# Performance work log

Hardware: AMD Instinct MI355X
Metric: run time of the kernel (lower is better)

Reference implementation:

```python
import jax, jax.numpy as jnp
import numpy as np

B, S, DIM = 2, 2048, 4096
N_HEADS, N_KV_HEADS = 32, 8
HEAD_DIM = DIM // N_HEADS  # 128
N_REP = N_HEADS // N_KV_HEADS  # 4
NEG_INF = -1e9


def setup_inputs() -> dict:
    key = jax.random.key(0)
    ks = jax.random.split(key, 6)
    x = jax.random.normal(ks[0], (B, S, DIM), dtype=jnp.float32)
    # torch Linear weights are [out_features, in_features]
    sc = 0.02
    wq = jax.random.normal(ks[1], (N_HEADS * HEAD_DIM, DIM), dtype=jnp.float32) * sc
    wk = jax.random.normal(ks[2], (N_KV_HEADS * HEAD_DIM, DIM), dtype=jnp.float32) * sc
    wv = jax.random.normal(ks[3], (N_KV_HEADS * HEAD_DIM, DIM), dtype=jnp.float32) * sc
    wo = jax.random.normal(ks[4], (DIM, N_HEADS * HEAD_DIM), dtype=jnp.float32) * sc
    # RoPE frequencies, matching llama precompute_freqs_cis (theta=10000)
    inv = 1.0 / (10000.0 ** (np.arange(0, HEAD_DIM, 2, dtype=np.float32) / HEAD_DIM))
    t = np.arange(S, dtype=np.float32)
    freqs = np.outer(t, inv)  # [S, HEAD_DIM//2]
    freqs_cos = jnp.asarray(np.cos(freqs), dtype=jnp.float32)
    freqs_sin = jnp.asarray(np.sin(freqs), dtype=jnp.float32)
    # causal mask: 0 on/below diagonal, large negative above
    mask = jnp.triu(jnp.full((S, S), NEG_INF, dtype=jnp.float32), k=1)
    return {"x": x, "wq": wq, "wk": wk, "wv": wv, "wo": wo,
            "freqs_cos": freqs_cos, "freqs_sin": freqs_sin,
            "mask": mask, "start_pos": 0}


def _apply_rope(t, cos, sin):
    # t: [b, s, h, hd]; complex mult on interleaved (even, odd) pairs
    tr, ti = t[..., 0::2], t[..., 1::2]
    cos = cos[None, :, None, :]
    sin = sin[None, :, None, :]
    out_r = tr * cos - ti * sin
    out_i = tr * sin + ti * cos
    return jnp.stack([out_r, out_i], axis=-1).reshape(t.shape)


def reference(x, wq, wk, wv, wo, freqs_cos, freqs_sin, mask, start_pos):
    bsz, seqlen, _ = x.shape
    xq = (x @ wq.T).reshape(bsz, seqlen, N_HEADS, HEAD_DIM)
    xk = (x @ wk.T).reshape(bsz, seqlen, N_KV_HEADS, HEAD_DIM)
    xv = (x @ wv.T).reshape(bsz, seqlen, N_KV_HEADS, HEAD_DIM)
    xq = _apply_rope(xq, freqs_cos, freqs_sin)
    xk = _apply_rope(xk, freqs_cos, freqs_sin)
    # prefill: start_pos == 0, so cache slice == current keys/values
    # GQA repeat_kv via broadcast (torch repeat_interleave over head dim)
    keys = jnp.broadcast_to(xk[:, :, :, None, :],
                            (bsz, seqlen, N_KV_HEADS, N_REP, HEAD_DIM)
                            ).reshape(bsz, seqlen, N_HEADS, HEAD_DIM)
    values = jnp.broadcast_to(xv[:, :, :, None, :],
                              (bsz, seqlen, N_KV_HEADS, N_REP, HEAD_DIM)
                              ).reshape(bsz, seqlen, N_HEADS, HEAD_DIM)
    scale = 1.0 / jnp.sqrt(jnp.float32(HEAD_DIM))
    # [b, h, q, k]
    scores = jnp.einsum('bqhd,bkhd->bhqk', xq, keys) * scale
    scores = scores + mask[None, None, :, :]
    probs = jax.nn.softmax(scores.astype(jnp.float32), axis=-1).astype(xq.dtype)
    out = jnp.einsum('bhqk,bkhd->bqhd', probs, values)
    out = out.reshape(bsz, seqlen, N_HEADS * HEAD_DIM)
    return out @ wo.T
```

## Files before the change

### kernel.cpp

```cpp
#include <hip/hip_runtime.h>

typedef unsigned short u16;
typedef unsigned int u32;
typedef __bf16 bf16_t;
typedef bf16_t bf16x8 __attribute__((ext_vector_type(8)));
typedef float f32x4 __attribute__((ext_vector_type(4)));

#define B_ 2
#define S_ 2048
#define DIM_ 4096
#define NH_ 32
#define NKV_ 8
#define HD_ 128

__device__ __forceinline__ u16 f2b(float f) {
  union { float f; unsigned u; } x; x.f = f;
  unsigned r = x.u + 0x7fffu + ((x.u >> 16) & 1u);
  return (u16)(r >> 16);
}
__device__ __forceinline__ float b2f(u16 u) {
  union { unsigned u; float f; } x; x.u = ((unsigned)u) << 16;
  return x.f;
}
__device__ __forceinline__ u32 cvtpk(float lo, float hi) {
  u32 r;
  asm volatile("v_cvt_pk_bf16_f32 %0, %1, %2" : "=v"(r) : "v"(lo), "v"(hi));
  return r;
}
__device__ __forceinline__ float redmax4(float x) {
  x = fmaxf(x, __shfl_xor(x, 16));
  x = fmaxf(x, __shfl_xor(x, 32));
  return x;
}
__device__ __forceinline__ float redsum4(float x) {
  x += __shfl_xor(x, 16);
  x += __shfl_xor(x, 32);
  return x;
}

#define GLDS(gsrc, ldst) \
  __builtin_amdgcn_global_load_lds((const __attribute__((address_space(1))) void*)(gsrc), \
                                   (__attribute__((address_space(3))) void*)(ldst), 16, 0, 0)
#define BAR()    __builtin_amdgcn_s_barrier()
#define SCHED0() __builtin_amdgcn_sched_barrier(0)

__global__ void cvt_kernel(const float* __restrict__ in, u16* __restrict__ out, int n4) {
  int i = blockIdx.x * blockDim.x + threadIdx.x;
  int stride = gridDim.x * blockDim.x;
  for (; i < n4; i += stride) {
    float4 v = ((const float4*)in)[i];
    ushort4 o;
    o.x = f2b(v.x); o.y = f2b(v.y); o.z = f2b(v.z); o.w = f2b(v.w);
    ((ushort4*)out)[i] = o;
  }
}

__global__ void rope_kernel(u16* __restrict__ t, const float* __restrict__ fc,
                            const float* __restrict__ fs, int nheads) {
  int idx = blockIdx.x * blockDim.x + threadIdx.x;
  int ppr = nheads * 64;
  int row = idx / ppr;
  int pr = idx - row * ppr;
  int h = pr >> 6, j = pr & 63;
  int s = row & (S_ - 1);
  float c = fc[s * 64 + j], sn = fs[s * 64 + j];
  u16* p = t + (size_t)row * (size_t)(nheads * HD_) + h * HD_ + j * 2;
  float tr = b2f(p[0]), ti = b2f(p[1]);
  p[0] = f2b(tr * c - ti * sn);
  p[1] = f2b(tr * sn + ti * c);
}

template<int MODE, bool SM>
__global__ __launch_bounds__(512, 2) void gemm256(const u16* __restrict__ A,
                                                  const u16* __restrict__ B,
                                                  void* __restrict__ Cout,
                                                  void* __restrict__ Cout2,
                                                  int M, int N, int K) {
  constexpr int BM = SM ? 128 : 256;
  constexpr int AH = SM ? 4096 : 8192;
  constexpr int II = SM ? 1 : 2;
  constexpr int NACC = SM ? 4 : 8;
  __shared__ u16 As[2][2][AH];
  __shared__ u16 Bs[2][2][8192];
  const int nbn = N >> 8;
  const int nwg = gridDim.x;
  int wg = blockIdx.x;
  wg = (wg & 7) * (nwg >> 3) + (wg >> 3);
  const int bm = wg / nbn;
  const int bn = wg - bm * nbn;
  const int tid = threadIdx.x;
  const int lane = tid & 63;
  const int wv = tid >> 6;
  const int wm = wv >> 2, wn = wv & 3;
  const int qloc = lane & 15, grp = lane >> 4;
  const int NT = K >> 6;

  f32x4 acc[NACC][4];
#pragma unroll
  for (int i = 0; i < NACC; i++)
#pragma unroll
    for (int j = 0; j < 4; j++)
#pragma unroll
      for (int r = 0; r < 4; r++) acc[i][j][r] = 0.0f;

  const int srowl = lane >> 3;
  const int scsw = 8 * ((lane & 7) ^ srowl);
  const size_t rowA = SM ? ((size_t)(bm * 128 + wv * 8 + srowl) * K + scsw)
                         : ((size_t)(bm * 256 + wv * 16 + srowl) * K + scsw);
  const size_t rowB = (size_t)(bn * 256 + wv * 16 + srowl) * K + scsw;

#define STAGE_A(buf, h, tt) { \
    if (SM) { \
      GLDS(A + rowA + (size_t)((h) * 64) * K + (size_t)(tt) * 64, &As[buf][h][wv * 512]); \
    } else { \
      GLDS(A + rowA + (size_t)((h) * 128) * K + (size_t)(tt) * 64, &As[buf][h][wv * 1024]); \
      GLDS(A + rowA + (size_t)((h) * 128 + 8) * K + (size_t)(tt) * 64, &As[buf][h][wv * 1024 + 512]); } }
#define STAGE_B(buf, h, tt) { \
    GLDS(B + rowB + (size_t)((h) * 128) * K + (size_t)(tt) * 64, &Bs[buf][h][wv * 1024]); \
    GLDS(B + rowB + (size_t)((h) * 128 + 8) * K + (size_t)(tt) * 64, &Bs[buf][h][wv * 1024 + 512]); }

  STAGE_A(0, 0, 0); STAGE_A(0, 1, 0);
  STAGE_B(0, 0, 0); STAGE_B(0, 1, 0);
  STAGE_B(1, 0, 1); STAGE_B(1, 1, 1);
  asm volatile("s_waitcnt vmcnt(4)" ::: "memory");
  BAR();

  for (int t = 0; t < NT; t += 2) {
#pragma unroll
    for (int half = 0; half < 2; half++) {
      bf16x8 bfr[4][2];
#pragma unroll
      for (int qd = 0; qd < 4; qd++) {
        if (qd == 0) {
#pragma unroll
          for (int j = 0; j < 4; j++)
#pragma unroll
            for (int ks = 0; ks < 2; ks++) {
              int rb = (wn & 1) * 64 + j * 16 + qloc;
              bfr[j][ks] = *(const bf16x8*)((const char*)&Bs[half][wn >> 1][0]
                           + rb * 128 + ((ks * 64 + grp * 16) ^ ((rb & 7) << 4)));
            }
        }
        bf16x8 af[II][2];
#pragma unroll
        for (int ii = 0; ii < II; ii++)
#pragma unroll
          for (int ks = 0; ks < 2; ks++) {
            int rh = SM ? (qd * 16 + qloc) : (qd * 32 + ii * 16 + qloc);
            af[ii][ks] = *(const bf16x8*)((const char*)&As[half][wm][0]
                         + rh * 128 + ((ks * 64 + grp * 16) ^ ((rh & 7) << 4)));
          }
        const int ph = half * 4 + qd;
        if (ph == 0)      { STAGE_A(1, 0, t + 1); }
        else if (ph == 1) { STAGE_A(1, 1, t + 1); }
        else if (ph == 2) { if (t + 2 < NT) STAGE_B(0, 0, t + 2); }
        else if (ph == 3) { if (t + 2 < NT) STAGE_B(0, 1, t + 2); }
        else if (ph == 4) { if (t + 2 < NT) STAGE_A(0, 0, t + 2); }
        else if (ph == 5) { if (t + 2 < NT) STAGE_A(0, 1, t + 2); }
        else if (ph == 6) { if (t + 3 < NT) STAGE_B(1, 0, t + 3); }
        else              { if (t + 3 < NT) STAGE_B(1, 1, t + 3); }
        BAR();
        __builtin_amdgcn_s_setprio(1);
#pragma unroll
        for (int ii = 0; ii < II; ii++)
#pragma unroll
          for (int ks = 0; ks < 2; ks++)
#pragma unroll
            for (int j = 0; j < 4; j++)
              acc[qd * II + ii][j] = __builtin_amdgcn_mfma_f32_16x16x32_bf16(
                  af[ii][ks], bfr[j][ks], acc[qd * II + ii][j], 0, 0, 0);
        __builtin_amdgcn_s_setprio(0);
        SCHED0();
        if (qd == 3) {
          if ((half == 0 ? t + 2 : t + 3) < NT)
            asm volatile("s_waitcnt vmcnt(4)" ::: "memory");
          else
            asm volatile("s_waitcnt vmcnt(0)" ::: "memory");
        }
        BAR();
      }
    }
  }
#undef STAGE_A
#undef STAGE_B

  const int r0g = bm * BM + wm * (BM / 2) + grp * 4;
  const int c0g = bn * 256 + wn * 64 + qloc;
#pragma unroll
  for (int i = 0; i < NACC; i++)
#pragma unroll
    for (int j = 0; j < 4; j++)
#pragma unroll
      for (int r = 0; r < 4; r++) {
        int row = r0g + i * 16 + r;
        int col = c0g + j * 16;
        float v = acc[i][j][r];
        if (MODE == 1)      ((float*)Cout)[(size_t)row * N + col] = v;
        else if (MODE == 0) ((u16*)Cout)[(size_t)row * N + col]  = f2b(v);
        else {
          if (col < 1024) ((u16*)Cout)[(size_t)row * 1024 + col] = f2b(v);
          else            ((u16*)Cout2)[(size_t)(col - 1024) * M + row] = f2b(v);
        }
      }
}

__global__ __launch_bounds__(512) void attn_kernel(const u16* __restrict__ Q,
                                                   const u16* __restrict__ Kt,
                                                   const u16* __restrict__ VT,
                                                   u16* __restrict__ O,
                                                   const float* __restrict__ fc,
                                                   const float* __restrict__ fs) {
  __shared__ u16 Ks[2][32 * 128];
  __shared__ u16 Vs[2][32 * 128];

  const int bid = blockIdx.x;
  const int qb = 15 - (bid >> 6);
  const int h = bid & 31;
  const int b = (bid >> 5) & 1;
  const int g = h >> 2;
  const int tid = threadIdx.x;
  const int lane = tid & 63;
  const int wv = tid >> 6;
  const int qrow0 = qb * 128 + wv * 16;
  const float scl2 = 0.12751744f;

  const int qloc = lane & 15;
  const int grp = lane >> 4;

  bf16x8 qf[4];
  {
    const int qr = qrow0 + qloc;
    const u16* qptr = Q + (size_t)(b * S_ + qr) * (NH_ * HD_) + h * HD_ + grp * 8;
#pragma unroll
    for (int c = 0; c < 4; c++) {
      union { bf16x8 v; u16 u[8]; } raw;
      raw.v = *(const bf16x8*)(qptr + c * 32);
      const int p0 = c * 16 + grp * 4;
      const float4 cv = *(const float4*)&fc[(size_t)qr * 64 + p0];
      const float4 sv = *(const float4*)&fs[(size_t)qr * 64 + p0];
      union { bf16x8 v; u32 w[4]; } out;
      const float cc[4] = {cv.x, cv.y, cv.z, cv.w};
      const float ss[4] = {sv.x, sv.y, sv.z, sv.w};
#pragma unroll
      for (int j = 0; j < 4; j++) {
        float tr = b2f(raw.u[2 * j]), ti = b2f(raw.u[2 * j + 1]);
        out.w[j] = cvtpk(tr * cc[j] - ti * ss[j], tr * ss[j] + ti * cc[j]);
      }
      qf[c] = out.v;
    }
  }

  float m = -1e30f, l = 0.f;
  f32x4 o[8];
#pragma unroll
  for (int c = 0; c < 8; c++)
#pragma unroll
    for (int r = 0; r < 4; r++) o[c][r] = 0.f;

  const int nkv = 4 * qb + 4;

  int ka[2][4];
#pragma unroll
  for (int n = 0; n < 2; n++)
#pragma unroll
    for (int c = 0; c < 4; c++) {
      int krow = n * 16 + qloc;
      ka[n][c] = krow * 256 + ((c * 64 + grp * 16) ^ ((krow & 7) << 4));
    }
  int va[8];
#pragma unroll
  for (int c = 0; c < 8; c++) {
    int d = c * 16 + qloc;
    va[c] = d * 64 + ((grp * 16) ^ (((d >> 1) & 3) << 4));
  }

  const int kkey = wv * 4 + grp;
  const int cbsK = (qloc * 16) ^ ((kkey & 7) << 4);
  const int vd = wv * 16 + (lane >> 2);
  const int kbsV = ((lane & 3) * 16) ^ (((vd >> 1) & 3) << 4);

  const u16* kp = Kt + (size_t)(b * S_ + kkey) * 1024 + g * HD_ + (cbsK >> 1);
  const u16* vp = VT + (size_t)(g * HD_ + vd) * 4096 + (size_t)b * S_ + (kbsV >> 1);

  GLDS(kp, &Ks[0][wv * 512]);
  GLDS(vp, &Vs[0][wv * 512]);
  kp += 32 * 1024;
  vp += 32;

#define ATTN_ITER(T, CB, NB)                                                   \
  {                                                                            \
    const bool pf = ((T) + 1 < nkv);                                           \
    if (pf) {                                                                  \
      GLDS(kp, &Ks[NB][wv * 512]);                                             \
      GLDS(vp, &Vs[NB][wv * 512]);                                             \
      asm volatile("s_waitcnt vmcnt(2)" ::: "memory");                         \
    } else {                                                                   \
      asm volatile("s_waitcnt vmcnt(0)" ::: "memory");                         \
    }                                                                          \
    BAR();                                                                     \
    SCHED0();                                                                  \
    if ((T) * 32 <= qrow0 + 15) {                                              \
      f32x4 s[2];                                                              \
      __builtin_amdgcn_s_setprio(1);                                           \
      _Pragma("unroll")                                                        \
      for (int n = 0; n < 2; n++) {                                            \
        f32x4 sc;                                                              \
        _Pragma("unroll")                                                      \
        for (int r = 0; r < 4; r++) sc[r] = 0.f;                               \
        _Pragma("unroll")                                                      \
        for (int c = 0; c < 4; c++) {                                          \
          bf16x8 kf = *(const bf16x8*)((const char*)Ks[CB] + ka[n][c]);        \
          sc = __builtin_amdgcn_mfma_f32_16x16x32_bf16(kf, qf[c], sc, 0, 0, 0);\
        }                                                                      \
        s[n] = sc;                                                             \
      }                                                                        \
      __builtin_amdgcn_s_setprio(0);                                           \
      const int q = qrow0 + qloc;                                              \
      if ((T) * 32 + 31 > qrow0) {                                             \
        _Pragma("unroll")                                                      \
        for (int n = 0; n < 2; n++)                                            \
          _Pragma("unroll")                                                    \
          for (int r = 0; r < 4; r++) {                                        \
            int k = (T) * 32 + n * 16 + grp * 4 + r;                           \
            if (k > q) s[n][r] = -1e9f;                                        \
          }                                                                    \
      }                                                                        \
      float pmax = fmaxf(fmaxf(fmaxf(s[0][0], s[0][1]), fmaxf(s[0][2], s[0][3])), \
                         fmaxf(fmaxf(s[1][0], s[1][1]), fmaxf(s[1][2], s[1][3]))); \
      pmax = redmax4(pmax);                                                    \
      if (__any(pmax > m + 64.f)) {                                            \
        float mn = fmaxf(m, pmax);                                             \
        float alpha = exp2f((m - mn) * scl2);                                  \
        m = mn;                                                                \
        l *= alpha;                                                            \
        float ar[4];                                                           \
        _Pragma("unroll")                                                      \
        for (int r = 0; r < 4; r++) ar[r] = __shfl(alpha, grp * 4 + r);        \
        _Pragma("unroll")                                                      \
        for (int c = 0; c < 8; c++)                                            \
          _Pragma("unroll")                                                    \
          for (int r = 0; r < 4; r++) o[c][r] *= ar[r];                        \
      }                                                                        \
      const float msc = m * scl2;                                              \
      float p[2][4];                                                           \
      _Pragma("unroll")                                                        \
      for (int n = 0; n < 2; n++)                                              \
        _Pragma("unroll")                                                      \
        for (int r = 0; r < 4; r++)                                            \
          p[n][r] = exp2f(fmaf(s[n][r], scl2, -msc));                          \
      float rs = ((p[0][0] + p[0][1]) + (p[0][2] + p[0][3])) +                 \
                 ((p[1][0] + p[1][1]) + (p[1][2] + p[1][3]));                  \
      l += redsum4(rs);                                                        \
      u32 a0 = cvtpk(p[0][0], p[0][1]);                                        \
      u32 a1 = cvtpk(p[0][2], p[0][3]);                                        \
      u32 b0 = cvtpk(p[1][0], p[1][1]);                                        \
      u32 b1 = cvtpk(p[1][2], p[1][3]);                                        \
      asm volatile("v_permlane32_swap_b32 %0, %1" : "+v"(a0), "+v"(b0));       \
      asm volatile("v_permlane32_swap_b32 %0, %1" : "+v"(a1), "+v"(b1));       \
      asm volatile("v_permlane16_swap_b32 %0, %1" : "+v"(a0), "+v"(b0));       \
      asm volatile("v_permlane16_swap_b32 %0, %1" : "+v"(a1), "+v"(b1));       \
      union { bf16x8 v; u32 w[4]; } pau;                                       \
      pau.w[0] = a0; pau.w[1] = a1; pau.w[2] = b0; pau.w[3] = b1;              \
      bf16x8 pa = pau.v;                                                       \
      __builtin_amdgcn_s_setprio(1);                                           \
      _Pragma("unroll")                                                        \
      for (int c = 0; c < 8; c++) {                                            \
        bf16x8 vf = *(const bf16x8*)((const char*)Vs[CB] + va[c]);             \
        o[c] = __builtin_amdgcn_mfma_f32_16x16x32_bf16(pa, vf, o[c], 0, 0, 0); \
      }                                                                        \
      __builtin_amdgcn_s_setprio(0);                                           \
    }                                                                          \
    asm volatile("s_waitcnt lgkmcnt(0)" ::: "memory");                         \
    SCHED0();                                                                  \
    BAR();                                                                     \
    kp += 32 * 1024;                                                           \
    vp += 32;                                                                  \
  }

  for (int t = 0; t < nkv; t += 2) {
    ATTN_ITER(t, 0, 1);
    ATTN_ITER(t + 1, 1, 0);
  }
#undef ATTN_ITER

  float lr[4];
#pragma unroll
  for (int r = 0; r < 4; r++) lr[r] = 1.0f / __shfl(l, grp * 4 + r);
#pragma unroll
  for (int c = 0; c < 8; c++)
#pragma unroll
    for (int r = 0; r < 4; r++) {
      int qo = qrow0 + grp * 4 + r;
      float val = o[c][r] * lr[r];
      O[(size_t)(b * S_ + qo) * (NH_ * HD_) + h * HD_ + c * 16 + qloc] = f2b(val);
    }
}

extern "C" void kernel_launch(void* const* d_in, const int* in_sizes, int n_in,
                              void* d_out, int out_size, void* d_ws, size_t ws_size,
                              hipStream_t stream) {
  const float* x  = (const float*)d_in[0];
  const float* wq = (const float*)d_in[1];
  const float* wk = (const float*)d_in[2];
  const float* wv = (const float*)d_in[3];
  const float* wo = (const float*)d_in[4];
  const float* fc = (const float*)d_in[5];
  const float* fs = (const float*)d_in[6];

  char* ws = (char*)d_ws;
  u16* Xb  = (u16*)(ws);
  u16* Wqb = (u16*)(ws + 33554432);
  u16* Wkv = (u16*)(ws + 67108864);
  u16* Qw  = (u16*)(ws + 83886080);
  u16* Kw  = (u16*)(ws + 117440512);
  u16* Vw  = (u16*)(ws + 125829120);
  u16* Ow  = Xb;
  u16* Wob = Wqb;

  auto cvt = [&](const float* in, u16* out, int n) {
    int n4 = n >> 2;
    int blocks = (n4 + 255) / 256; if (blocks > 2048) blocks = 2048;
    cvt_kernel<<<dim3(blocks), dim3(256), 0, stream>>>(in, out, n4);
  };
  cvt(x,  Xb,  B_ * S_ * DIM_);
  cvt(wq, Wqb, DIM_ * DIM_);
  cvt(wk, Wkv, NKV_ * HD_ * DIM_);
  cvt(wv, Wkv + (size_t)1024 * 4096, NKV_ * HD_ * DIM_);

  gemm256<0, false><<<dim3(16 * 16), 512, 0, stream>>>(Xb, Wqb, Qw, nullptr, 4096, 4096, 4096);
  gemm256<3, true><<<dim3(32 * 8), 512, 0, stream>>>(Xb, Wkv, Kw, Vw, 4096, 2048, 4096);

  cvt(wo, Wob, DIM_ * DIM_);

  rope_kernel<<<dim3((B_ * S_ * NKV_ * 64) / 256), 256, 0, stream>>>(Kw, fc, fs, NKV_);

  attn_kernel<<<dim3(B_ * NH_ * (S_ / 128)), 512, 0, stream>>>(Qw, Kw, Vw, Ow, fc, fs);

  gemm256<1, false><<<dim3(16 * 16), 512, 0, stream>>>(Ow, Wob, d_out, nullptr, 4096, 4096, 4096);
}
```

Measured before the change: 514.3 us.

## Double per-wave query rows in attention to reuse K/V LDS fragments

Each wave now handles 32 query rows as two 16-row fragments instead of 16, so the attention block covers 256 queries and the grid is halved. Every K and V fragment read from LDS feeds two MFMAs, which halves LDS traffic and global K/V loads per query. The cost is doubled accumulator registers (launch bounds now request occupancy 4), half as many blocks (512 on the device), and coarser causal tiles that add wasted masked work and load imbalance.

Result: slower. 705.3 us (+37.1%).

```diff
diff --git a/kernel.cpp b/kernel.cpp
--- a/kernel.cpp
+++ b/kernel.cpp
@@ -204,32 +204,33 @@
       }
 }
 
-__global__ __launch_bounds__(512) void attn_kernel(const u16* __restrict__ Q,
-                                                   const u16* __restrict__ Kt,
-                                                   const u16* __restrict__ VT,
-                                                   u16* __restrict__ O,
-                                                   const float* __restrict__ fc,
-                                                   const float* __restrict__ fs) {
+__global__ __launch_bounds__(512, 4) void attn_kernel(const u16* __restrict__ Q,
+                                                      const u16* __restrict__ Kt,
+                                                      const u16* __restrict__ VT,
+                                                      u16* __restrict__ O,
+                                                      const float* __restrict__ fc,
+                                                      const float* __restrict__ fs) {
   __shared__ u16 Ks[2][32 * 128];
   __shared__ u16 Vs[2][32 * 128];
 
   const int bid = blockIdx.x;
-  const int qb = 15 - (bid >> 6);
+  const int qb = 7 - (bid >> 6);
   const int h = bid & 31;
   const int b = (bid >> 5) & 1;
   const int g = h >> 2;
   const int tid = threadIdx.x;
   const int lane = tid & 63;
   const int wv = tid >> 6;
-  const int qrow0 = qb * 128 + wv * 16;
+  const int qrow0 = qb * 256 + wv * 32;
   const float scl2 = 0.12751744f;
 
   const int qloc = lane & 15;
   const int grp = lane >> 4;
 
-  bf16x8 qf[4];
-  {
-    const int qr = qrow0 + qloc;
+  bf16x8 qf[2][4];
+#pragma unroll
+  for (int f = 0; f < 2; f++) {
+    const int qr = qrow0 + f * 16 + qloc;
     const u16* qptr = Q + (size_t)(b * S_ + qr) * (NH_ * HD_) + h * HD_ + grp * 8;
 #pragma unroll
     for (int c = 0; c < 4; c++) {
@@ -246,18 +247,20 @@
         float tr = b2f(raw.u[2 * j]), ti = b2f(raw.u[2 * j + 1]);
         out.w[j] = cvtpk(tr * cc[j] - ti * ss[j], tr * ss[j] + ti * cc[j]);
       }
-      qf[c] = out.v;
+      qf[f][c] = out.v;
     }
   }
 
-  float m = -1e30f, l = 0.f;
-  f32x4 o[8];
-#pragma unroll
-  for (int c = 0; c < 8; c++)
-#pragma unroll
-    for (int r = 0; r < 4; r++) o[c][r] = 0.f;
-
-  const int nkv = 4 * qb + 4;
+  float m[2] = {-1e30f, -1e30f}, l[2] = {0.f, 0.f};
+  f32x4 o[2][8];
+#pragma unroll
+  for (int f = 0; f < 2; f++)
+#pragma unroll
+    for (int c = 0; c < 8; c++)
+#pragma unroll
+      for (int r = 0; r < 4; r++) o[f][c][r] = 0.f;
+
+  const int nkv = 8 * qb + 8;
 
   int ka[2][4];
 #pragma unroll
@@ -299,74 +302,93 @@
     }                                                                          \
     BAR();                                                                     \
     SCHED0();                                                                  \
-    if ((T) * 32 <= qrow0 + 15) {                                              \
-      f32x4 s[2];                                                              \
+    if ((T) * 32 <= qrow0 + 31) {                                              \
+      f32x4 s[2][2];                                                           \
+      _Pragma("unroll")                                                        \
+      for (int f = 0; f < 2; f++)                                              \
+        _Pragma("unroll")                                                      \
+        for (int n = 0; n < 2; n++)                                            \
+          _Pragma("unroll")                                                    \
+          for (int r = 0; r < 4; r++) s[f][n][r] = 0.f;                        \
       __builtin_amdgcn_s_setprio(1);                                           \
       _Pragma("unroll")                                                        \
       for (int n = 0; n < 2; n++) {                                            \
-        f32x4 sc;                                                              \
-        _Pragma("unroll")                                                      \
-        for (int r = 0; r < 4; r++) sc[r] = 0.f;                               \
         _Pragma("unroll")                                                      \
         for (int c = 0; c < 4; c++) {                                          \
           bf16x8 kf = *(const bf16x8*)((const char*)Ks[CB] + ka[n][c]);        \
-          sc = __builtin_amdgcn_mfma_f32_16x16x32_bf16(kf, qf[c], sc, 0, 0, 0);\
+          s[0][n] = __builtin_amdgcn_mfma_f32_16x16x32_bf16(kf, qf[0][c], s[0][n], 0, 0, 0); \
+          s[1][n] = __builtin_amdgcn_mfma_f32_16x16x32_bf16(kf, qf[1][c], s[1][n], 0, 0, 0); \
         }                                                                      \
-        s[n] = sc;                                                             \
       }                                                                        \
       __builtin_amdgcn_s_setprio(0);                                           \
-      const int q = qrow0 + qloc;                                              \
       if ((T) * 32 + 31 > qrow0) {                                             \
+        _Pragma("unroll")                                                      \
+        for (int f = 0; f < 2; f++) {                                          \
+          const int q = qrow0 + f * 16 + qloc;                                 \
+          _Pragma("unroll")                                                    \
+          for (int n = 0; n < 2; n++)                                          \
+            _Pragma("unroll")                                                  \
+            for (int r = 0; r < 4; r++) {                                      \
+              int k = (T) * 32 + n * 16 + grp * 4 + r;                         \
+              if (k > q) s[f][n][r] = -1e9f;                                   \
+            }                                                                  \
+        }                                                                      \
+      }                                                                        \
+      float pmax[2];                                                           \
+      _Pragma("unroll")                                                        \
+      for (int f = 0; f < 2; f++) {                                            \
+        pmax[f] = fmaxf(fmaxf(fmaxf(s[f][0][0], s[f][0][1]), fmaxf(s[f][0][2], s[f][0][3])), \
+                        fmaxf(fmaxf(s[f][1][0], s[f][1][1]), fmaxf(s[f][1][2], s[f][1][3]))); \
+        pmax[f] = redmax4(pmax[f]);                                            \
+      }                                                                        \
+      bool need = (pmax[0] > m[0] + 64.f) || (pmax[1] > m[1] + 64.f);          \
+      if (__any(need)) {                                                       \
+        _Pragma("unroll")                                                      \
+        for (int f = 0; f < 2; f++) {                                          \
+          float mn = fmaxf(m[f], pmax[f]);                                     \
+          float alpha = exp2f((m[f] - mn) * scl2);                             \
+          m[f] = mn;                                                           \
+          l[f] *= alpha;                                                       \
+          float ar[4];                                                         \
+          _Pragma("unroll")                                                    \
+          for (int r = 0; r < 4; r++) ar[r] = __shfl(alpha, grp * 4 + r);      \
+          _Pragma("unroll")                                                    \
+          for (int c = 0; c < 8; c++)                                          \
+            _Pragma("unroll")                                                  \
+            for (int r = 0; r < 4; r++) o[f][c][r] *= ar[r];                   \
+        }                                                                      \
+      }                                                                        \
+      bf16x8 pa[2];                                                            \
+      _Pragma("unroll")                                                        \
+      for (int f = 0; f < 2; f++) {                                            \
+        const float msc = m[f] * scl2;                                         \
+        float p[2][4];                                                         \
         _Pragma("unroll")                                                      \
         for (int n = 0; n < 2; n++)                                            \
           _Pragma("unroll")                                                    \
-          for (int r = 0; r < 4; r++) {                                        \
-            int k = (T) * 32 + n * 16 + grp * 4 + r;                           \
-            if (k > q) s[n][r] = -1e9f;                                        \
-          }                                                                    \
-      }                                                                        \
-      float pmax = fmaxf(fmaxf(fmaxf(s[0][0], s[0][1]), fmaxf(s[0][2], s[0][3])), \
-                         fmaxf(fmaxf(s[1][0], s[1][1]), fmaxf(s[1][2], s[1][3]))); \
-      pmax = redmax4(pmax);                                                    \
-      if (__any(pmax > m + 64.f)) {                                            \
-        float mn = fmaxf(m, pmax);                                             \
-        float alpha = exp2f((m - mn) * scl2);                                  \
-        m = mn;                                                                \
-        l *= alpha;                                                            \
-        float ar[4];                                                           \
-        _Pragma("unroll")                                                      \
-        for (int r = 0; r < 4; r++) ar[r] = __shfl(alpha, grp * 4 + r);        \
-        _Pragma("unroll")                                                      \
-        for (int c = 0; c < 8; c++)                                            \
-          _Pragma("unroll")                                                    \
-          for (int r = 0; r < 4; r++) o[c][r] *= ar[r];                        \
-      }                                                                        \
-      const float msc = m * scl2;                                              \
-      float p[2][4];                                                           \
-      _Pragma("unroll")                                                        \
-      for (int n = 0; n < 2; n++)                                              \
-        _Pragma("unroll")                                                      \
-        for (int r = 0; r < 4; r++)                                            \
-          p[n][r] = exp2f(fmaf(s[n][r], scl2, -msc));                          \
-      float rs = ((p[0][0] + p[0][1]) + (p[0][2] + p[0][3])) +                 \
-                 ((p[1][0] + p[1][1]) + (p[1][2] + p[1][3]));                  \
-      l += redsum4(rs);                                                        \
-      u32 a0 = cvtpk(p[0][0], p[0][1]);                                        \
-      u32 a1 = cvtpk(p[0][2], p[0][3]);                                        \
-      u32 b0 = cvtpk(p[1][0], p[1][1]);                                        \
-      u32 b1 = cvtpk(p[1][2], p[1][3]);                                        \
-      asm volatile("v_permlane32_swap_b32 %0, %1" : "+v"(a0), "+v"(b0));       \
-      asm volatile("v_permlane32_swap_b32 %0, %1" : "+v"(a1), "+v"(b1));       \
-      asm volatile("v_permlane16_swap_b32 %0, %1" : "+v"(a0), "+v"(b0));       \
-      asm volatile("v_permlane16_swap_b32 %0, %1" : "+v"(a1), "+v"(b1));       \
-      union { bf16x8 v; u32 w[4]; } pau;                                       \
-      pau.w[0] = a0; pau.w[1] = a1; pau.w[2] = b0; pau.w[3] = b1;              \
-      bf16x8 pa = pau.v;                                                       \
+          for (int r = 0; r < 4; r++)                                          \
+            p[n][r] = exp2f(fmaf(s[f][n][r], scl2, -msc));                     \
+        float rs = ((p[0][0] + p[0][1]) + (p[0][2] + p[0][3])) +               \
+                   ((p[1][0] + p[1][1]) + (p[1][2] + p[1][3]));                \
+        l[f] += redsum4(rs);                                                   \
+        u32 a0 = cvtpk(p[0][0], p[0][1]);                                      \
+        u32 a1 = cvtpk(p[0][2], p[0][3]);                                      \
+        u32 b0 = cvtpk(p[1][0], p[1][1]);                                      \
+        u32 b1 = cvtpk(p[1][2], p[1][3]);                                      \
+        asm volatile("v_permlane32_swap_b32 %0, %1" : "+v"(a0), "+v"(b0));     \
+        asm volatile("v_permlane32_swap_b32 %0, %1" : "+v"(a1), "+v"(b1));     \
+        asm volatile("v_permlane16_swap_b32 %0, %1" : "+v"(a0), "+v"(b0));     \
+        asm volatile("v_permlane16_swap_b32 %0, %1" : "+v"(a1), "+v"(b1));     \
+        union { bf16x8 v; u32 w[4]; } pau;                                     \
+        pau.w[0] = a0; pau.w[1] = a1; pau.w[2] = b0; pau.w[3] = b1;            \
+        pa[f] = pau.v;                                                         \
+      }                                                                        \
       __builtin_amdgcn_s_setprio(1);                                           \
       _Pragma("unroll")                                                        \
       for (int c = 0; c < 8; c++) {                                            \
         bf16x8 vf = *(const bf16x8*)((const char*)Vs[CB] + va[c]);             \
-        o[c] = __builtin_amdgcn_mfma_f32_16x16x32_bf16(pa, vf, o[c], 0, 0, 0); \
+        o[0][c] = __builtin_amdgcn_mfma_f32_16x16x32_bf16(pa[0], vf, o[0][c], 0, 0, 0); \
+        o[1][c] = __builtin_amdgcn_mfma_f32_16x16x32_bf16(pa[1], vf, o[1][c], 0, 0, 0); \
       }                                                                        \
       __builtin_amdgcn_s_setprio(0);                                           \
     }                                                                          \
@@ -383,17 +405,20 @@
   }
 #undef ATTN_ITER
 
-  float lr[4];
-#pragma unroll
-  for (int r = 0; r < 4; r++) lr[r] = 1.0f / __shfl(l, grp * 4 + r);
-#pragma unroll
-  for (int c = 0; c < 8; c++)
-#pragma unroll
-    for (int r = 0; r < 4; r++) {
-      int qo = qrow0 + grp * 4 + r;
-      float val = o[c][r] * lr[r];
-      O[(size_t)(b * S_ + qo) * (NH_ * HD_) + h * HD_ + c * 16 + qloc] = f2b(val);
-    }
+#pragma unroll
+  for (int f = 0; f < 2; f++) {
+    float lr[4];
+#pragma unroll
+    for (int r = 0; r < 4; r++) lr[r] = 1.0f / __shfl(l[f], grp * 4 + r);
+#pragma unroll
+    for (int c = 0; c < 8; c++)
+#pragma unroll
+      for (int r = 0; r < 4; r++) {
+        int qo = qrow0 + f * 16 + grp * 4 + r;
+        float val = o[f][c][r] * lr[r];
+        O[(size_t)(b * S_ + qo) * (NH_ * HD_) + h * HD_ + c * 16 + qloc] = f2b(val);
+      }
+  }
 }
 
 extern "C" void kernel_launch(void* const* d_in, const int* in_sizes, int n_in,
@@ -434,7 +459,7 @@
 
   rope_kernel<<<dim3((B_ * S_ * NKV_ * 64) / 256), 256, 0, stream>>>(Kw, fc, fs, NKV_);
 
-  attn_kernel<<<dim3(B_ * NH_ * (S_ / 128)), 512, 0, stream>>>(Qw, Kw, Vw, Ow, fc, fs);
+  attn_kernel<<<dim3(B_ * NH_ * (S_ / 256)), 512, 0, stream>>>(Qw, Kw, Vw, Ow, fc, fs);
 
   gemm256<1, false><<<dim3(16 * 16), 512, 0, stream>>>(Ow, Wob, d_out, nullptr, 4096, 4096, 4096);
 }
```
